# Kernel optimization log

Measured on AMD Instinct MI355X. Metric: run time of the kernel, lower is better.

Reference implementation:

```python
import jax, jax.numpy as jnp
import numpy as np

EMBED = 1024
HEADS = 16
HEAD_DIM = EMBED // HEADS
HIDDEN = 4096
EPS = 1e-5


def setup_inputs() -> dict:
    key = jax.random.key(0)
    ks = jax.random.split(key, 16)
    s_e = 1.0 / np.sqrt(EMBED)
    s_h = 1.0 / np.sqrt(HIDDEN)
    return {
        "x": jax.random.normal(ks[0], (8, 1024, EMBED), dtype=jnp.float32),
        "ln1_g": jnp.ones((EMBED,), jnp.float32),
        "ln1_b": jnp.zeros((EMBED,), jnp.float32),
        "ln2_g": jnp.ones((EMBED,), jnp.float32),
        "ln2_b": jnp.zeros((EMBED,), jnp.float32),
        "wq": jax.random.uniform(ks[1], (EMBED, EMBED), jnp.float32, -s_e, s_e),
        "bq": jax.random.uniform(ks[2], (EMBED,), jnp.float32, -s_e, s_e),
        "wk": jax.random.uniform(ks[3], (EMBED, EMBED), jnp.float32, -s_e, s_e),
        "bk": jax.random.uniform(ks[4], (EMBED,), jnp.float32, -s_e, s_e),
        "wv": jax.random.uniform(ks[5], (EMBED, EMBED), jnp.float32, -s_e, s_e),
        "bv": jax.random.uniform(ks[6], (EMBED,), jnp.float32, -s_e, s_e),
        "wo": jax.random.uniform(ks[7], (EMBED, EMBED), jnp.float32, -s_e, s_e),
        "bo": jax.random.uniform(ks[8], (EMBED,), jnp.float32, -s_e, s_e),
        "w1": jax.random.uniform(ks[9], (EMBED, HIDDEN), jnp.float32, -s_e, s_e),
        "b1": jax.random.uniform(ks[10], (HIDDEN,), jnp.float32, -s_e, s_e),
        "w2": jax.random.uniform(ks[11], (HIDDEN, EMBED), jnp.float32, -s_h, s_h),
        "b2": jax.random.uniform(ks[12], (EMBED,), jnp.float32, -s_h, s_h),
    }


def _layernorm(x, g, b):
    mu = jnp.mean(x, axis=-1, keepdims=True)
    var = jnp.mean((x - mu) ** 2, axis=-1, keepdims=True)
    return (x - mu) * jax.lax.rsqrt(var + EPS) * g + b


def reference(x, ln1_g, ln1_b, ln2_g, ln2_b, wq, bq, wk, bk, wv, bv, wo, bo, w1, b1, w2, b2):
    B, N, E = x.shape
    scale = HEAD_DIM ** (-0.5)
    # --- attention sublayer (pre-norm) ---
    h = _layernorm(x, ln1_g, ln1_b)
    q = (h @ wq + bq).reshape(B, N, HEADS, HEAD_DIM).transpose(0, 2, 1, 3) * scale
    k = (h @ wk + bk).reshape(B, N, HEADS, HEAD_DIM).transpose(0, 2, 1, 3)
    v = (h @ wv + bv).reshape(B, N, HEADS, HEAD_DIM).transpose(0, 2, 1, 3)
    scores = jnp.einsum("bhqd,bhkd->bhqk", q, k)
    attn = jax.nn.softmax(scores, axis=-1)
    ctx = jnp.einsum("bhqk,bhkd->bhqd", attn, v)
    ctx = ctx.transpose(0, 2, 1, 3).reshape(B, N, E)
    x = x + (ctx @ wo + bo)
    # --- FFN sublayer (pre-norm) ---
    h2 = _layernorm(x, ln2_g, ln2_b)
    ff = jax.nn.relu(h2 @ w1 + b1) @ w2 + b2
    return x + ff
```

## Files before the change

### kernel.cpp

```cpp
#include <hip/hip_runtime.h>
#include <hip/hip_bf16.h>

typedef __attribute__((ext_vector_type(4))) float f32x4;
typedef __attribute__((ext_vector_type(16))) float f32x16;
typedef __attribute__((ext_vector_type(8))) __bf16 bf16x8;
typedef __attribute__((ext_vector_type(4))) __bf16 bf16x4;
typedef __attribute__((ext_vector_type(4))) unsigned int u32x4;

static constexpr int E    = 1024;
static constexpr int TOK  = 8192;
static constexpr int HID  = 4096;

#define DEVINL __device__ __forceinline__

DEVINL void gload16(const void* g, void* l) {
  __builtin_amdgcn_global_load_lds((__attribute__((address_space(1))) void*)g,
                                   (__attribute__((address_space(3))) void*)l, 16, 0, 0);
}

#define ABAR()  asm volatile("s_barrier" ::: "memory")
#define AVM(n)  asm volatile("s_waitcnt vmcnt(" #n ")" ::: "memory")
#define ALGKM0() asm volatile("s_waitcnt lgkmcnt(0)")
#define CVTPK(dst, lo, hi) asm("v_cvt_pk_bf16_f32 %0, %1, %2" : "=v"(dst) : "v"(lo), "v"(hi))
#define PLSWAP(a, b) asm("v_permlane32_swap_b32 %0, %1" : "+v"(a), "+v"(b))

template <int N> DEVINL void avm() {
  if constexpr (N == 0)      asm volatile("s_waitcnt vmcnt(0)" ::: "memory");
  else if constexpr (N == 1) asm volatile("s_waitcnt vmcnt(1)" ::: "memory");
  else if constexpr (N == 2) asm volatile("s_waitcnt vmcnt(2)" ::: "memory");
  else if constexpr (N == 6) asm volatile("s_waitcnt vmcnt(6)" ::: "memory");
  else                       asm volatile("s_waitcnt vmcnt(0)" ::: "memory");
}

__global__ __launch_bounds__(256) void wconv6_kernel(const float* __restrict__ wq,
                                                     const float* __restrict__ wk,
                                                     const float* __restrict__ wv,
                                                     const float* __restrict__ wo,
                                                     const float* __restrict__ w1,
                                                     const float* __restrict__ w2,
                                                     __bf16* __restrict__ Wqkv,
                                                     __bf16* __restrict__ Wot,
                                                     __bf16* __restrict__ W1t,
                                                     __bf16* __restrict__ W2t) {
  const int id = blockIdx.x;
  const float* W; __bf16* Wt; int K, N, lid;
  if (id < 1024)      { W = wq; Wt = Wqkv;                K = 1024; N = 1024; lid = id; }
  else if (id < 2048) { W = wk; Wt = Wqkv + 1024 * 1024;  K = 1024; N = 1024; lid = id - 1024; }
  else if (id < 3072) { W = wv; Wt = Wqkv + 2048 * 1024;  K = 1024; N = 1024; lid = id - 2048; }
  else if (id < 4096) { W = wo; Wt = Wot;                 K = 1024; N = 1024; lid = id - 3072; }
  else if (id < 8192) { W = w1; Wt = W1t;                 K = 1024; N = 4096; lid = id - 4096; }
  else                { W = w2; Wt = W2t;                 K = 4096; N = 1024; lid = id - 8192; }
  const int nx = N >> 5;
  const long n0 = (long)(lid % nx) * 32;
  const long k0 = (long)(lid / nx) * 32;

  __shared__ float tile[32][33];
  const int t  = threadIdx.x;
  const int r  = t >> 3;
  const int c4 = (t & 7) * 4;
  float4 v = *(const float4*)&W[(k0 + r) * N + n0 + c4];
  tile[r][c4 + 0] = v.x; tile[r][c4 + 1] = v.y;
  tile[r][c4 + 2] = v.z; tile[r][c4 + 3] = v.w;
  __syncthreads();
  bf16x4 o;
#pragma unroll
  for (int i = 0; i < 4; ++i) o[i] = (__bf16)tile[c4 + i][r];
  *(bf16x4*)&Wt[(n0 + r) * K + k0 + c4] = o;
}

__global__ __launch_bounds__(256) void ln_kernel(const float* __restrict__ X,
                                                 const float* __restrict__ g,
                                                 const float* __restrict__ be,
                                                 __bf16* __restrict__ O) {
  const int t = threadIdx.x;
  const long row = blockIdx.x;
  float4 v = *(const float4*)&X[row * E + t * 4];
  float s  = v.x + v.y + v.z + v.w;
  float ss = v.x * v.x + v.y * v.y + v.z * v.z + v.w * v.w;
#pragma unroll
  for (int off = 32; off; off >>= 1) {
    s  += __shfl_down(s, off);
    ss += __shfl_down(ss, off);
  }
  __shared__ float red[8];
  const int w = t >> 6;
  if ((t & 63) == 0) { red[w] = s; red[4 + w] = ss; }
  __syncthreads();
  s  = red[0] + red[1] + red[2] + red[3];
  ss = red[4] + red[5] + red[6] + red[7];
  const float mean = s * (1.0f / E);
  const float var  = ss * (1.0f / E) - mean * mean;
  const float rstd = rsqrtf(var + 1e-5f);
  float4 gv = *(const float4*)&g[t * 4];
  float4 bv = *(const float4*)&be[t * 4];
  bf16x4 o;
  o[0] = (__bf16)((v.x - mean) * rstd * gv.x + bv.x);
  o[1] = (__bf16)((v.y - mean) * rstd * gv.y + bv.y);
  o[2] = (__bf16)((v.z - mean) * rstd * gv.z + bv.z);
  o[3] = (__bf16)((v.w - mean) * rstd * gv.w + bv.w);
  *(bf16x4*)&O[row * E + t * 4] = o;
}

__global__ __launch_bounds__(256) void reduce2_kernel(float* __restrict__ out,
                                                      const __bf16* __restrict__ t0,
                                                      const __bf16* __restrict__ t1,
                                                      const float* __restrict__ b2) {
  const int i = blockIdx.x * 256 + threadIdx.x;
  float4 o = ((const float4*)out)[i];
  bf16x4 a = ((const bf16x4*)t0)[i];
  bf16x4 b = ((const bf16x4*)t1)[i];
  float4 bb = ((const float4*)b2)[i & 255];
  o.x += bb.x + (float)a[0] + (float)b[0];
  o.y += bb.y + (float)a[1] + (float)b[1];
  o.z += bb.z + (float)a[2] + (float)b[2];
  o.w += bb.w + (float)a[3] + (float)b[3];
  ((float4*)out)[i] = o;
}

template <bool RELU, bool RESID, bool OUTBF, int NB>
__global__ __launch_bounds__(512, 2) void gemm8p_kernel(const __bf16* __restrict__ A,
                                                        const __bf16* __restrict__ Bt,
                                                        const float* __restrict__ bias0,
                                                        const float* __restrict__ bias1,
                                                        const float* __restrict__ bias2,
                                                        const float* resid,
                                                        void* Cout, void* Cout2,
                                                        int M, int N, int K, int KLD) {
  extern __shared__ char lds[];
  const int tid  = threadIdx.x;
  const int lane = tid & 63;
  const int l15  = lane & 15;
  const int kp   = lane >> 4;
  const int wid  = tid >> 6;
  const int wr   = wid >> 2;
  const int wc   = wid & 3;

  const int gx   = gridDim.x, gy = gridDim.y;
  const int nwg  = gx * gy * gridDim.z;
  const int flat = blockIdx.x + gx * (blockIdx.y + gy * blockIdx.z);
  const int swz  = (flat & 7) * (nwg >> 3) + (flat >> 3);
  const int bx   = swz % gx;
  const int by   = (swz / gx) % gy;
  const int bz   = swz / (gx * gy);
  const long brow = (long)by * 256;
  const long bcol = (long)bx * 256;
  const long koff = (long)bz * K;

  const __bf16* Ab = A  + brow * KLD + koff;
  const __bf16* Bb = Bt + bcol * KLD + koff;
  void* Cdst = bz ? Cout2 : Cout;
  const int NT = K >> 6;

  auto stageU = [&](const __bf16* Gb, int rc0, int k0, int dstOff) {
#pragma unroll
    for (int i = 0; i < 2; ++i) {
      const int c = i * 512 + tid;
      const int r = c >> 3;
      const int p = (c & 7) ^ (r & 7);
      gload16(Gb + (long)(rc0 + r) * KLD + k0 + p * 8, lds + dstOff + c * 16);
    }
  };

  f32x4 acc[8][4];
  const f32x4 z4 = {0.f, 0.f, 0.f, 0.f};
#pragma unroll
  for (int m = 0; m < 8; ++m)
#pragma unroll
    for (int n = 0; n < 4; ++n) acc[m][n] = z4;

  bf16x8 af[4][2], bh0[2][2], bh1[2][2];

  auto readA = [&](int off) {
#pragma unroll
    for (int mm = 0; mm < 4; ++mm)
#pragma unroll
      for (int kk = 0; kk < 2; ++kk) {
        const int lr = mm * 32 + wr * 16 + l15;
        const int p  = ((kk << 2) + kp) ^ (lr & 7);
        af[mm][kk] = *(const bf16x8*)(lds + off + lr * 128 + p * 16);
      }
  };
  auto readB = [&](int off, bf16x8 (*bf)[2]) {
#pragma unroll
    for (int nn = 0; nn < 2; ++nn)
#pragma unroll
      for (int kk = 0; kk < 2; ++kk) {
        const int lc = nn * 64 + wc * 16 + l15;
        const int p  = ((kk << 2) + kp) ^ (lc & 7);
        bf[nn][kk] = *(const bf16x8*)(lds + off + lc * 128 + p * 16);
      }
  };
  auto quad = [&](int mb, int nb, bf16x8 (*bf)[2]) {
    __builtin_amdgcn_s_setprio(1);
#pragma unroll
    for (int kk = 0; kk < 2; ++kk)
#pragma unroll
      for (int mm = 0; mm < 4; ++mm)
#pragma unroll
        for (int nn = 0; nn < 2; ++nn)
          acc[mb + mm][nb + nn] = __builtin_amdgcn_mfma_f32_16x16x32_bf16(
              af[mm][kk], bf[nn][kk], acc[mb + mm][nb + nn], 0, 0, 0);
    __builtin_amdgcn_s_setprio(0);
  };

  stageU(Ab, 0,   0, 0);
  stageU(Bb, 0,   0, 32768);
  stageU(Bb, 128, 0, 49152);
  stageU(Ab, 128, 0, 16384);
  stageU(Ab, 0,   64, 65536 + 0);
  stageU(Bb, 0,   64, 65536 + 32768);
  stageU(Bb, 128, 64, 65536 + 49152);
  avm<6>();
  ABAR();

  for (int t = 0; t < NT; ++t) {
    const int cb  = (t & 1) ? 65536 : 0;
    const int nb1 = cb ^ 65536;
    const int k1 = (t + 1 < NT) ? ((t + 1) << 6) : 0;
    const int k2 = (t + 2 < NT) ? ((t + 2) << 6) : 0;

    readA(cb + 0);
    readB(cb + 32768, bh0);
    stageU(Ab, 128, k1, nb1 + 16384);
    ABAR(); ALGKM0();
    quad(0, 0, bh0);
    ABAR();

    readB(cb + 49152, bh1);
    stageU(Ab, 0, k2, cb + 0);
    ABAR(); ALGKM0();
    quad(0, 2, bh1);
    ABAR();

    readA(cb + 16384);
    stageU(Bb, 0, k2, cb + 32768);
    ABAR(); ALGKM0();
    quad(4, 0, bh0);
    ABAR();

    stageU(Bb, 128, k2, cb + 49152);
    avm<6>();
    ABAR();
    quad(4, 2, bh1);
    ABAR();
  }
  avm<0>();

#pragma unroll
  for (int m = 0; m < 8; ++m) {
#pragma unroll
    for (int n = 0; n < 4; ++n) {
      const long col = bcol + n * 64 + wc * 16 + l15;
      float bb;
      if (NB == 3) {
        const float* bp = (col < 1024) ? bias0 : ((col < 2048) ? bias1 : bias2);
        bb = bp[col & 1023];
      } else if (NB == 1) {
        bb = bias0[col];
      } else {
        bb = 0.f;
      }
#pragma unroll
      for (int j = 0; j < 4; ++j) {
        const long row = brow + m * 32 + wr * 16 + (lane >> 4) * 4 + j;
        float val = acc[m][n][j] + bb;
        if (RELU) val = fmaxf(val, 0.f);
        const long idx = row * N + col;
        if (RESID) val += resid[idx];
        if (OUTBF) ((__bf16*)Cdst)[idx] = (__bf16)val;
        else       ((float*)Cdst)[idx]  = val;
      }
    }
  }
}

template <int BM_, int DEPTH, bool RELU, bool RESID, bool OUTBF, int NB>
__global__ __launch_bounds__(512, 2) void gemmk_kernel(const __bf16* __restrict__ A,
                                                       const __bf16* __restrict__ Bt,
                                                       const float* __restrict__ bias0,
                                                       const float* __restrict__ bias1,
                                                       const float* __restrict__ bias2,
                                                       const float* resid,
                                                       void* Cout, void* Cout2,
                                                       int M, int N, int K, int KLD) {
  extern __shared__ char lds[];
  constexpr int MF    = BM_ / 32;
  constexpr int ABYT  = BM_ * 64;
  constexpr int TILEB = ABYT + 16384;
  constexpr int AL    = BM_ / 128;
  constexpr int TL    = AL + 2;
  constexpr int W     = (DEPTH - 2) * TL;

  const int tid  = threadIdx.x;
  const int lane = tid & 63;
  const int l15  = lane & 15;
  const int kp   = lane >> 4;
  const int wid  = tid >> 6;
  const int wr   = wid >> 2;
  const int wc   = wid & 3;

  const int gx   = gridDim.x, gy = gridDim.y;
  const int nwg  = gx * gy * gridDim.z;
  const int flat = blockIdx.x + gx * (blockIdx.y + gy * blockIdx.z);
  const int swz  = (flat & 7) * (nwg >> 3) + (flat >> 3);
  const int bx   = swz % gx;
  const int by   = (swz / gx) % gy;
  const int bz   = swz / (gx * gy);
  const long brow = (long)by * BM_;
  const long bcol = (long)bx * 256;
  const long koff = (long)bz * K;

  const __bf16* Ab = A  + brow * KLD + koff;
  const __bf16* Bb = Bt + bcol * KLD + koff;
  void* Cdst = bz ? Cout2 : Cout;
  const int NT = K >> 5;

  auto stageA = [&](int k0, char* dst) {
#pragma unroll
    for (int i = 0; i < AL; ++i) {
      const int c = i * 512 + tid;
      const int r = c >> 2;
      const int p = (c & 3) ^ ((r >> 1) & 3);
      gload16(Ab + (long)r * KLD + k0 + p * 8, dst + c * 16);
    }
  };
  auto stageB = [&](int k0, char* dst) {
#pragma unroll
    for (int i = 0; i < 2; ++i) {
      const int c = i * 512 + tid;
      const int r = c >> 2;
      const int p = (c & 3) ^ ((r >> 1) & 3);
      gload16(Bb + (long)r * KLD + k0 + p * 8, dst + c * 16);
    }
  };

  f32x4 acc[MF][4];
  const f32x4 z4 = {0.f, 0.f, 0.f, 0.f};
#pragma unroll
  for (int m = 0; m < MF; ++m)
#pragma unroll
    for (int n = 0; n < 4; ++n) acc[m][n] = z4;

#pragma unroll
  for (int pt = 0; pt < DEPTH - 1; ++pt) {
    stageA(pt * 32, lds + pt * TILEB);
    stageB(pt * 32, lds + pt * TILEB + ABYT);
  }

  bf16x8 af[4], bfr[4];

  for (int t = 0; t < NT; ++t) {
    const int cb = t % DEPTH;
    const int sb = (t + DEPTH - 1) % DEPTH;
    const char* Ac = lds + cb * TILEB;
    const char* Bc = Ac + ABYT;
    char* An = lds + sb * TILEB;
    const int kt = (t + DEPTH - 1 < NT) ? ((t + DEPTH - 1) << 5) : 0;

    avm<W>();
    ABAR();

#pragma unroll
    for (int m = 0; m < 4; ++m) {
      const int row = m * 32 + wr * 16 + l15;
      af[m] = *(const bf16x8*)(Ac + row * 64 + (kp ^ ((row >> 1) & 3)) * 16);
    }
#pragma unroll
    for (int n = 0; n < 4; ++n) {
      const int col = n * 64 + wc * 16 + l15;
      bfr[n] = *(const bf16x8*)(Bc + col * 64 + (kp ^ ((col >> 1) & 3)) * 16);
    }
    stageA(kt, An);
    stageB(kt, An + ABYT);
    ABAR(); ALGKM0();
    __builtin_amdgcn_s_setprio(1);
#pragma unroll
    for (int m = 0; m < 4; ++m)
#pragma unroll
      for (int n = 0; n < 4; ++n)
        acc[m][n] = __builtin_amdgcn_mfma_f32_16x16x32_bf16(af[m], bfr[n], acc[m][n], 0, 0, 0);
    __builtin_amdgcn_s_setprio(0);
  }
  avm<0>();

#pragma unroll
  for (int m = 0; m < MF; ++m) {
#pragma unroll
    for (int n = 0; n < 4; ++n) {
      const long col = bcol + n * 64 + wc * 16 + l15;
      float bb;
      if (NB == 3) {
        const float* bp = (col < 1024) ? bias0 : ((col < 2048) ? bias1 : bias2);
        bb = bp[col & 1023];
      } else if (NB == 1) {
        bb = bias0[col];
      } else {
        bb = 0.f;
      }
#pragma unroll
      for (int j = 0; j < 4; ++j) {
        const long row = brow + m * 32 + wr * 16 + (lane >> 4) * 4 + j;
        float val = acc[m][n][j] + bb;
        if (RELU) val = fmaxf(val, 0.f);
        const long idx = row * N + col;
        if (RESID) val += resid[idx];
        if (OUTBF) ((__bf16*)Cdst)[idx] = (__bf16)val;
        else       ((float*)Cdst)[idx]  = val;
      }
    }
  }
}

__global__ __launch_bounds__(512, 2) void attn_kernel(const __bf16* __restrict__ QKV,
                                                      __bf16* __restrict__ Og) {
  __shared__ __align__(16) char alds[32768];

  const int QSTR = 3072;
  const int t    = threadIdx.x;
  const int lane = t & 63;
  const int w    = t >> 6;
  const int l31  = lane & 31;
  const int h    = lane >> 5;
  const int b    = blockIdx.y >> 4;
  const int hh   = blockIdx.y & 15;
  const long row0 = (long)b * 1024 + (long)blockIdx.x * 256;
  const long kvrow0 = (long)b * 1024;
  const int colQ = hh * 64;
  const int colK = colQ + 1024;
  const int colV = colQ + 2048;

  char* const KsB = alds;
  char* const VtB = alds + 16384;

#pragma unroll
  for (int j = 0; j < 4; ++j) {
    const int c = j * 512 + t;
    const int r = c >> 3;
    const int p = (c & 7) ^ (r & 7);
    gload16(QKV + (row0 + r) * QSTR + colQ + p * 8, alds + c * 16);
  }
  AVM(0);
  __syncthreads();
  bf16x8 bq[4];
  {
    const int qrow = w * 32 + l31;
#pragma unroll
    for (int kk = 0; kk < 4; ++kk) {
      const int p = (kk * 2 + h) ^ (qrow & 7);
      bq[kk] = *(const bf16x8*)(alds + qrow * 128 + p * 16);
    }
  }
  ALGKM0();
  __syncthreads();

  {
    const int c = t;
    const int r = c >> 3;
    const int p = (c & 7) ^ (r & 7);
    gload16(QKV + (kvrow0 + r) * QSTR + colK + p * 8, KsB + c * 16);
  }
  bf16x8 vv;
  {
    const int key = t >> 3, dc = t & 7;
    vv = *(const bf16x8*)(QKV + (kvrow0 + key) * QSTR + colV + dc * 8);
  }
  AVM(0);
  {
    const int key = t >> 3, dc = t & 7;
#pragma unroll
    for (int e = 0; e < 8; ++e) {
      const int d = dc * 8 + e;
      const int pc = ((key >> 3) ^ dc ^ e) & 7;
      *(__bf16*)(VtB + d * 128 + pc * 16 + (key & 7) * 2) = vv[e];
    }
  }
  __syncthreads();

  f32x16 ctx0, ctx1;
#pragma unroll
  for (int r = 0; r < 16; ++r) { ctx0[r] = 0.f; ctx1[r] = 0.f; }
  float m = -INFINITY, l = 0.f;
  const float K2 = 0.1803368801f;

  for (int kb = 0; kb < 16; ++kb) {
    const int cur = kb & 1, nxt = cur ^ 1;
    const int kb1 = (kb + 1 < 16) ? kb + 1 : kb;
    const long kr1 = kvrow0 + kb1 * 64;
    const char* KsC = KsB + cur * 8192;
    const char* VtC = VtB + cur * 8192;

    {
      const int key = t >> 3, dc = t & 7;
      vv = *(const bf16x8*)(QKV + (kr1 + key) * QSTR + colV + dc * 8);
    }
    {
      const int c = t;
      const int r = c >> 3;
      const int p = (c & 7) ^ (r & 7);
      gload16(QKV + (kr1 + r) * QSTR + colK + p * 8, KsB + nxt * 8192 + c * 16);
    }

    f32x16 s0, s1;
#pragma unroll
    for (int r = 0; r < 16; ++r) { s0[r] = 0.f; s1[r] = 0.f; }
    __builtin_amdgcn_s_setprio(1);
#pragma unroll
    for (int kk = 0; kk < 4; ++kk) {
      const int pce = kk * 2 + h;
      const int p0i = pce ^ (l31 & 7);
      bf16x8 ak0 = *(const bf16x8*)(KsC + l31 * 128 + p0i * 16);
      bf16x8 ak1 = *(const bf16x8*)(KsC + (32 + l31) * 128 + p0i * 16);
      s0 = __builtin_amdgcn_mfma_f32_32x32x16_bf16(ak0, bq[kk], s0, 0, 0, 0);
      s1 = __builtin_amdgcn_mfma_f32_32x32x16_bf16(ak1, bq[kk], s1, 0, 0, 0);
    }
    __builtin_amdgcn_s_setprio(0);

    float ma = fmaxf(fmaxf(s0[0], s0[1]), s0[2]);
    float mb = fmaxf(fmaxf(s0[3], s0[4]), s0[5]);
    float mc = fmaxf(fmaxf(s0[6], s0[7]), s0[8]);
    float md = fmaxf(fmaxf(s0[9], s0[10]), s0[11]);
    ma = fmaxf(fmaxf(ma, s0[12]), s0[13]);
    mb = fmaxf(fmaxf(mb, s0[14]), s0[15]);
    mc = fmaxf(fmaxf(mc, s1[0]), s1[1]);
    md = fmaxf(fmaxf(md, s1[2]), s1[3]);
    ma = fmaxf(fmaxf(ma, s1[4]), s1[5]);
    mb = fmaxf(fmaxf(mb, s1[6]), s1[7]);
    mc = fmaxf(fmaxf(mc, s1[8]), s1[9]);
    md = fmaxf(fmaxf(md, s1[10]), s1[11]);
    ma = fmaxf(fmaxf(ma, s1[12]), s1[13]);
    mb = fmaxf(fmaxf(mb, s1[14]), s1[15]);
    float mx = fmaxf(fmaxf(ma, mb), fmaxf(mc, md));
    mx = fmaxf(mx, __shfl_xor(mx, 32));

    if (!__all(mx - m <= 64.f)) {
      const float mn = fmaxf(m, mx);
      const float corr = exp2f((m - mn) * K2);
      l *= corr;
#pragma unroll
      for (int r = 0; r < 16; ++r) { ctx0[r] *= corr; ctx1[r] *= corr; }
      m = mn;
    }
    const float mK2 = m * K2;
    f32x16 p0, p1;
    float r0 = 0.f, r1 = 0.f, r2 = 0.f, r3 = 0.f;
#pragma unroll
    for (int r = 0; r < 16; r += 4) {
      p0[r + 0] = exp2f(fmaf(s0[r + 0], K2, -mK2)); r0 += p0[r + 0];
      p0[r + 1] = exp2f(fmaf(s0[r + 1], K2, -mK2)); r1 += p0[r + 1];
      p0[r + 2] = exp2f(fmaf(s0[r + 2], K2, -mK2)); r2 += p0[r + 2];
      p0[r + 3] = exp2f(fmaf(s0[r + 3], K2, -mK2)); r3 += p0[r + 3];
    }
#pragma unroll
    for (int r = 0; r < 16; r += 4) {
      p1[r + 0] = exp2f(fmaf(s1[r + 0], K2, -mK2)); r0 += p1[r + 0];
      p1[r + 1] = exp2f(fmaf(s1[r + 1], K2, -mK2)); r1 += p1[r + 1];
      p1[r + 2] = exp2f(fmaf(s1[r + 2], K2, -mK2)); r2 += p1[r + 2];
      p1[r + 3] = exp2f(fmaf(s1[r + 3], K2, -mK2)); r3 += p1[r + 3];
    }
    float rs = (r0 + r1) + (r2 + r3);
    rs += __shfl_xor(rs, 32);
    l += rs;

    AVM(1);
    {
      const int key = t >> 3, dc = t & 7;
      char* VtN = VtB + nxt * 8192;
#pragma unroll
      for (int e = 0; e < 8; ++e) {
        const int d = dc * 8 + e;
        const int pc = ((key >> 3) ^ dc ^ e) & 7;
        *(__bf16*)(VtN + d * 128 + pc * 16 + (key & 7) * 2) = vv[e];
      }
    }

    bf16x8 paf[4];
#pragma unroll
    for (int ks = 0; ks < 4; ++ks) {
      const int base = (ks & 1) * 8;
      unsigned a0, a1, b0, b1;
      if (ks < 2) {
        CVTPK(a0, p0[base + 0], p0[base + 1]);
        CVTPK(b0, p0[base + 4], p0[base + 5]);
        CVTPK(a1, p0[base + 2], p0[base + 3]);
        CVTPK(b1, p0[base + 6], p0[base + 7]);
      } else {
        CVTPK(a0, p1[base + 0], p1[base + 1]);
        CVTPK(b0, p1[base + 4], p1[base + 5]);
        CVTPK(a1, p1[base + 2], p1[base + 3]);
        CVTPK(b1, p1[base + 6], p1[base + 7]);
      }
      PLSWAP(a0, b0);
      PLSWAP(a1, b1);
      u32x4 wv4; wv4[0] = a0; wv4[1] = a1; wv4[2] = b0; wv4[3] = b1;
      paf[ks] = __builtin_bit_cast(bf16x8, wv4);
    }

    __builtin_amdgcn_s_setprio(1);
#pragma unroll
    for (int ks = 0; ks < 4; ++ks) {
      const int pce = ks * 2 + h;
      const int pA = (pce ^ (l31 >> 3) ^ (l31 & 7)) & 7;
      const int pB = (pce ^ (4 + (l31 >> 3)) ^ (l31 & 7)) & 7;
      bf16x8 av0 = *(const bf16x8*)(VtC + l31 * 128 + pA * 16);
      bf16x8 av1 = *(const bf16x8*)(VtC + (32 + l31) * 128 + pB * 16);
      ctx0 = __builtin_amdgcn_mfma_f32_32x32x16_bf16(av0, paf[ks], ctx0, 0, 0, 0);
      ctx1 = __builtin_amdgcn_mfma_f32_32x32x16_bf16(av1, paf[ks], ctx1, 0, 0, 0);
    }
    __builtin_amdgcn_s_setprio(0);

    __syncthreads();
  }

  const float inv = 1.0f / l;
  const long orow = row0 + w * 32 + l31;
#pragma unroll
  for (int f = 0; f < 2; ++f)
#pragma unroll
    for (int tq = 0; tq < 4; ++tq) {
      bf16x4 o;
#pragma unroll
      for (int e = 0; e < 4; ++e) {
        const float v = (f ? ctx1[tq * 4 + e] : ctx0[tq * 4 + e]) * inv;
        o[e] = (__bf16)v;
      }
      const int col = colQ + f * 32 + tq * 8 + h * 4;
      *(bf16x4*)&Og[orow * E + col] = o;
    }
}

extern "C" void kernel_launch(void* const* d_in, const int* in_sizes, int n_in,
                              void* d_out, int out_size, void* d_ws, size_t ws_size,
                              hipStream_t stream) {
  const float* x     = (const float*)d_in[0];
  const float* ln1g  = (const float*)d_in[1];
  const float* ln1b  = (const float*)d_in[2];
  const float* ln2g  = (const float*)d_in[3];
  const float* ln2b  = (const float*)d_in[4];
  const float* wq    = (const float*)d_in[5];
  const float* bq    = (const float*)d_in[6];
  const float* wk    = (const float*)d_in[7];
  const float* bk    = (const float*)d_in[8];
  const float* wv    = (const float*)d_in[9];
  const float* bv    = (const float*)d_in[10];
  const float* wo    = (const float*)d_in[11];
  const float* bo    = (const float*)d_in[12];
  const float* w1    = (const float*)d_in[13];
  const float* b1    = (const float*)d_in[14];
  const float* w2    = (const float*)d_in[15];
  const float* b2    = (const float*)d_in[16];
  float* out = (float*)d_out;

  char* ws = (char*)d_ws;
  const size_t MB = 1024 * 1024;
  __bf16* Wqkv = (__bf16*)(ws + 0 * MB);
  __bf16* Wot  = (__bf16*)(ws + 6 * MB);
  __bf16* W1t  = (__bf16*)(ws + 8 * MB);
  __bf16* W2t  = (__bf16*)(ws + 16 * MB);
  __bf16* h    = (__bf16*)(ws + 24 * MB);
  __bf16* qkv  = (__bf16*)(ws + 40 * MB);
  __bf16* ctx  = (__bf16*)(ws + 88 * MB);
  __bf16* ff1  = (__bf16*)(ws + 40 * MB);
  __bf16* tmp0 = (__bf16*)(ws + 0 * MB);
  __bf16* tmp1 = (__bf16*)(ws + 24 * MB);

  const dim3 blk(256);
  const dim3 blk512(512);
  const size_t GLDS8P  = 131072;
  const size_t GLDS128 = 5 * (128 * 64 + 16384);

  wconv6_kernel<<<12288, blk, 0, stream>>>(wq, wk, wv, wo, w1, w2,
                                           Wqkv, Wot, W1t, W2t);

  ln_kernel<<<TOK, blk, 0, stream>>>(x, ln1g, ln1b, h);

  gemm8p_kernel<false, false, true, 3><<<dim3(3072 / 256, TOK / 256), blk512, GLDS8P, stream>>>(
      h, Wqkv, bq, bk, bv, nullptr, qkv, nullptr, TOK, 3072, E, E);

  attn_kernel<<<dim3(4, 128), blk512, 0, stream>>>(qkv, ctx);

  gemmk_kernel<128, 5, false, true, false, 1><<<dim3(E / 256, TOK / 128), blk512, GLDS128, stream>>>(
      ctx, Wot, bo, nullptr, nullptr, x, out, nullptr, TOK, E, E, E);

  ln_kernel<<<TOK, blk, 0, stream>>>(out, ln2g, ln2b, h);

  gemm8p_kernel<true, false, true, 1><<<dim3(HID / 256, TOK / 256), blk512, GLDS8P, stream>>>(
      h, W1t, b1, nullptr, nullptr, nullptr, ff1, nullptr, TOK, HID, E, E);

  gemm8p_kernel<false, false, true, 0><<<dim3(E / 256, TOK / 256, 2), blk512, GLDS8P, stream>>>(
      ff1, W2t, nullptr, nullptr, nullptr, nullptr, tmp0, tmp1, TOK, E, HID / 2, HID);

  reduce2_kernel<<<TOK * E / 1024, blk, 0, stream>>>(out, tmp0, tmp1, b2);
}
```

Baseline: 355.8 us.

## Shrink attention blocks to 256 threads and prefetch V two tiles ahead

The attention kernel now runs 256-thread blocks covering 128 query rows each, launching twice as many blocks with a launch bound of three blocks per CU. The V loads are issued two key blocks ahead into registers, and the end-of-iteration __syncthreads is replaced by a partial vmcnt/lgkmcnt wait plus a raw barrier. The aim is better latency hiding and occupancy in the attention stage. The cost is more register pressure from the double-buffered V registers and twice as many K/V tile loads overall, since each block reloads keys and values for fewer queries.

```diff
diff --git a/kernel.cpp b/kernel.cpp
--- a/kernel.cpp
+++ b/kernel.cpp
@@ -21,13 +21,14 @@
 #define ABAR()  asm volatile("s_barrier" ::: "memory")
 #define AVM(n)  asm volatile("s_waitcnt vmcnt(" #n ")" ::: "memory")
 #define ALGKM0() asm volatile("s_waitcnt lgkmcnt(0)")
+#define AVMLG(n) asm volatile("s_waitcnt vmcnt(" #n ") lgkmcnt(0)" ::: "memory")
 #define CVTPK(dst, lo, hi) asm("v_cvt_pk_bf16_f32 %0, %1, %2" : "=v"(dst) : "v"(lo), "v"(hi))
 #define PLSWAP(a, b) asm("v_permlane32_swap_b32 %0, %1" : "+v"(a), "+v"(b))
 
 template <int N> DEVINL void avm() {
   if constexpr (N == 0)      asm volatile("s_waitcnt vmcnt(0)" ::: "memory");
-  else if constexpr (N == 1) asm volatile("s_waitcnt vmcnt(1)" ::: "memory");
   else if constexpr (N == 2) asm volatile("s_waitcnt vmcnt(2)" ::: "memory");
+  else if constexpr (N == 4) asm volatile("s_waitcnt vmcnt(4)" ::: "memory");
   else if constexpr (N == 6) asm volatile("s_waitcnt vmcnt(6)" ::: "memory");
   else                       asm volatile("s_waitcnt vmcnt(0)" ::: "memory");
 }
@@ -411,7 +412,7 @@
   }
 }
 
-__global__ __launch_bounds__(512, 2) void attn_kernel(const __bf16* __restrict__ QKV,
+__global__ __launch_bounds__(256, 3) void attn_kernel(const __bf16* __restrict__ QKV,
                                                       __bf16* __restrict__ Og) {
   __shared__ __align__(16) char alds[32768];
 
@@ -423,8 +424,8 @@
   const int h    = lane >> 5;
   const int b    = blockIdx.y >> 4;
   const int hh   = blockIdx.y & 15;
-  const long row0 = (long)b * 1024 + (long)blockIdx.x * 256;
-  const long kvrow0 = (long)b * 1024;
+  const long row0 = (long)b * 1024 + (long)blockIdx.x * 128;
+  const long kv0  = (long)b * 1024;
   const int colQ = hh * 64;
   const int colK = colQ + 1024;
   const int colV = colQ + 2048;
@@ -434,12 +435,12 @@
 
 #pragma unroll
   for (int j = 0; j < 4; ++j) {
-    const int c = j * 512 + t;
+    const int c = j * 256 + t;
     const int r = c >> 3;
     const int p = (c & 7) ^ (r & 7);
     gload16(QKV + (row0 + r) * QSTR + colQ + p * 8, alds + c * 16);
   }
-  AVM(0);
+  avm<0>();
   __syncthreads();
   bf16x8 bq[4];
   {
@@ -450,31 +451,41 @@
       bq[kk] = *(const bf16x8*)(alds + qrow * 128 + p * 16);
     }
   }
-  ALGKM0();
   __syncthreads();
 
-  {
-    const int c = t;
+#pragma unroll
+  for (int j = 0; j < 2; ++j) {
+    const int c = j * 256 + t;
     const int r = c >> 3;
     const int p = (c & 7) ^ (r & 7);
-    gload16(QKV + (kvrow0 + r) * QSTR + colK + p * 8, KsB + c * 16);
-  }
-  bf16x8 vv;
-  {
-    const int key = t >> 3, dc = t & 7;
-    vv = *(const bf16x8*)(QKV + (kvrow0 + key) * QSTR + colV + dc * 8);
-  }
-  AVM(0);
-  {
-    const int key = t >> 3, dc = t & 7;
+    gload16(QKV + (kv0 + r) * QSTR + colK + p * 8, KsB + c * 16);
+  }
+  bf16x8 vvP[2], vvN[2];
+#pragma unroll
+  for (int j = 0; j < 2; ++j) {
+    const int c = j * 256 + t;
+    const int key = c >> 3, dc = c & 7;
+    vvP[j] = *(const bf16x8*)(QKV + (kv0 + key) * QSTR + colV + dc * 8);
+  }
+  avm<0>();
+#pragma unroll
+  for (int j = 0; j < 2; ++j) {
+    const int c = j * 256 + t;
+    const int key = c >> 3, dc = c & 7;
 #pragma unroll
     for (int e = 0; e < 8; ++e) {
       const int d = dc * 8 + e;
       const int pc = ((key >> 3) ^ dc ^ e) & 7;
-      *(__bf16*)(VtB + d * 128 + pc * 16 + (key & 7) * 2) = vv[e];
+      *(__bf16*)(VtB + d * 128 + pc * 16 + (key & 7) * 2) = vvP[j][e];
     }
   }
   __syncthreads();
+#pragma unroll
+  for (int j = 0; j < 2; ++j) {
+    const int c = j * 256 + t;
+    const int key = c >> 3, dc = c & 7;
+    vvP[j] = *(const bf16x8*)(QKV + (kv0 + 64 + key) * QSTR + colV + dc * 8);
+  }
 
   f32x16 ctx0, ctx1;
 #pragma unroll
@@ -484,20 +495,23 @@
 
   for (int kb = 0; kb < 16; ++kb) {
     const int cur = kb & 1, nxt = cur ^ 1;
-    const int kb1 = (kb + 1 < 16) ? kb + 1 : kb;
-    const long kr1 = kvrow0 + kb1 * 64;
+    const int kb1 = (kb + 1 < 16) ? kb + 1 : 15;
+    const int kb2 = (kb + 2 < 16) ? kb + 2 : 15;
     const char* KsC = KsB + cur * 8192;
     const char* VtC = VtB + cur * 8192;
 
-    {
-      const int key = t >> 3, dc = t & 7;
-      vv = *(const bf16x8*)(QKV + (kr1 + key) * QSTR + colV + dc * 8);
-    }
-    {
-      const int c = t;
+#pragma unroll
+    for (int j = 0; j < 2; ++j) {
+      const int c = j * 256 + t;
       const int r = c >> 3;
       const int p = (c & 7) ^ (r & 7);
-      gload16(QKV + (kr1 + r) * QSTR + colK + p * 8, KsB + nxt * 8192 + c * 16);
+      gload16(QKV + (kv0 + kb1 * 64 + r) * QSTR + colK + p * 8, KsB + nxt * 8192 + c * 16);
+    }
+#pragma unroll
+    for (int j = 0; j < 2; ++j) {
+      const int c = j * 256 + t;
+      const int key = c >> 3, dc = c & 7;
+      vvN[j] = *(const bf16x8*)(QKV + (kv0 + kb2 * 64 + key) * QSTR + colV + dc * 8);
     }
 
     f32x16 s0, s1;
@@ -561,15 +575,19 @@
     rs += __shfl_xor(rs, 32);
     l += rs;
 
-    AVM(1);
+    avm<4>();
     {
-      const int key = t >> 3, dc = t & 7;
       char* VtN = VtB + nxt * 8192;
 #pragma unroll
-      for (int e = 0; e < 8; ++e) {
-        const int d = dc * 8 + e;
-        const int pc = ((key >> 3) ^ dc ^ e) & 7;
-        *(__bf16*)(VtN + d * 128 + pc * 16 + (key & 7) * 2) = vv[e];
+      for (int j = 0; j < 2; ++j) {
+        const int c = j * 256 + t;
+        const int key = c >> 3, dc = c & 7;
+#pragma unroll
+        for (int e = 0; e < 8; ++e) {
+          const int d = dc * 8 + e;
+          const int pc = ((key >> 3) ^ dc ^ e) & 7;
+          *(__bf16*)(VtN + d * 128 + pc * 16 + (key & 7) * 2) = vvP[j][e];
+        }
       }
     }
 
@@ -608,8 +626,12 @@
     }
     __builtin_amdgcn_s_setprio(0);
 
-    __syncthreads();
-  }
+    AVMLG(2);
+    ABAR();
+
+    vvP[0] = vvN[0]; vvP[1] = vvN[1];
+  }
+  avm<0>();
 
   const float inv = 1.0f / l;
   const long orow = row0 + w * 32 + l31;
@@ -676,7 +698,7 @@
   gemm8p_kernel<false, false, true, 3><<<dim3(3072 / 256, TOK / 256), blk512, GLDS8P, stream>>>(
       h, Wqkv, bq, bk, bv, nullptr, qkv, nullptr, TOK, 3072, E, E);
 
-  attn_kernel<<<dim3(4, 128), blk512, 0, stream>>>(qkv, ctx);
+  attn_kernel<<<dim3(8, 128), blk, 0, stream>>>(qkv, ctx);
 
   gemmk_kernel<128, 5, false, true, false, 1><<<dim3(E / 256, TOK / 128), blk512, GLDS128, stream>>>(
       ctx, Wot, bo, nullptr, nullptr, x, out, nullptr, TOK, E, E, E);
```

Result: no change. 356.4 us (+0.2%).
